# Kernel optimization log

Hardware: AMD Instinct MI355X
Metric: run time of the kernel (lower is better)

## Reference

```python
import jax, jax.numpy as jnp
import numpy as np

B, CIN, COUT, H, W = 64, 64, 64, 32, 32
K, STRIDE, PAD = 3, 1, 1
HOUT = (H + 2 * PAD - K) // STRIDE + 1
WOUT = (W + 2 * PAD - K) // STRIDE + 1


def setup_inputs() -> dict:
    key = jax.random.key(0)
    k1, k2, k3 = jax.random.split(key, 3)
    x = jax.random.normal(k1, (B, CIN, H, W), dtype=jnp.float32)
    # weight: per-location filters (leading singleton batch dim of the torch
    # param is dropped; it only served broadcasting)
    weight = jax.random.normal(k2, (CIN, COUT, HOUT, WOUT, K, K), dtype=jnp.float32)
    bias = jax.random.normal(k3, (COUT, HOUT, WOUT), dtype=jnp.float32)
    return {"x": x, "weight": weight, "bias": bias}


def _extract_patches(x, k, stride, pad, hout, wout):
    # x: [B, C, H, W] -> patches [B, C, k*k, hout, wout]
    xp = jnp.pad(x, ((0, 0), (0, 0), (pad, pad), (pad, pad)))
    slabs = [
        xp[:, :, i : i + (hout - 1) * stride + 1 : stride,
               j : j + (wout - 1) * stride + 1 : stride]
        for i in range(k) for j in range(k)
    ]
    return jnp.stack(slabs, axis=2)


def reference(x, weight, bias):
    cin, cout, hout, wout, k, _ = weight.shape
    patches = _extract_patches(x, k, STRIDE, PAD, hout, wout)  # [B, Cin, k*k, Ho, Wo]
    w = weight.reshape(cin, cout, hout, wout, k * k)
    # fused per-location dot product: avoids the [B,Cin,Cout,Ho,Wo,k,k] intermediate
    y = jnp.einsum('bikhw,iohwk->bohw', patches, w) + bias[None]
    return y
```

## Files before the change

### kernel.cpp

```cpp
#include <hip/hip_runtime.h>
#include <hip/hip_bf16.h>


#define B_    64
#define HW_   32
#define HP_   34
#define NLOC  1024
#define W_OST 9216u
#define W_IST 589824u
#define XT_BYTES  ((size_t)64*HP_*HP_*64*2)
#define WS_NEED   (XT_BYTES)
#define SCR_R 528

typedef __attribute__((ext_vector_type(8))) short short8;
typedef __attribute__((ext_vector_type(8))) unsigned short ushort8;
typedef __attribute__((ext_vector_type(4))) float floatx4;

static __device__ __forceinline__ unsigned short f2bf(float f) {
  __hip_bfloat16 h = __float2bfloat16(f);
  return __builtin_bit_cast(unsigned short, h);
}

static __device__ __forceinline__ void soft_barrier() {
  __asm__ volatile("s_waitcnt lgkmcnt(0)" ::: "memory");
  __builtin_amdgcn_s_barrier();
}

__global__ __launch_bounds__(256) void xpose_pad(const float* __restrict__ x,
                                                 unsigned short* __restrict__ xt) {
  int bid = blockIdx.x;
  int i = bid / HP_, hh = bid % HP_;
  __shared__ float tile[B_ * 33];
  int t = threadIdx.x;
  bool interior = (hh >= 1 && hh <= HW_);
  if (interior) {
    int h = hh - 1, w = t & 31, bs = t >> 5;
    #pragma unroll
    for (int r = 0; r < 8; ++r) {
      int b = r * 8 + bs;
      tile[b * 33 + w] = x[(((size_t)b * 64 + i) * HW_ + h) * HW_ + w];
    }
  }
  __syncthreads();
  int b = t & 63, wsb = t >> 6;
  size_t base = (size_t)(i * HP_ + hh) * HP_ * B_;
  #pragma unroll
  for (int s = 0; s < 9; ++s) {
    int ww = s * 4 + wsb;
    if (ww < HP_) {
      float v = 0.f;
      if (interior && ww >= 1 && ww <= HW_) v = tile[b * 33 + (ww - 1)];
      xt[base + (size_t)ww * B_ + b] = f2bf(v);
    }
  }
}

__global__ __launch_bounds__(256, 2) void lc2d_fused(
    const unsigned short* __restrict__ xt,
    const float* __restrict__ wsrc,
    const float* __restrict__ bias,
    float* __restrict__ out) {
  __shared__ __align__(16) unsigned short Bf[2][8 * 64 * 8];
  __shared__ __align__(16) unsigned short Bs[16 * 64 * 8];
  __shared__ __align__(16) unsigned short scr4[4][4 * SCR_R];

  const int bid   = blockIdx.x;
  const int lt    = ((bid & 7) << 6) | (bid >> 3);
  const int ohalf = lt & 1;
  const int loc0  = (lt >> 1) << 2;
  const int tid   = threadIdx.x;
  const int lane  = tid & 63;
  const int ll    = tid >> 6;
  const int loc   = loc0 + ll;
  const int hblk  = loc >> 5, wblk = loc & 31;
  const int col   = lane & 15;
  const int quad  = lane >> 4;
  const int o_0   = ohalf * 32 + col;

  floatx4 acc[4][2];
  {
    float b0 = bias[(unsigned)o_0 * 1024u + (unsigned)loc];
    float b1 = bias[(unsigned)(o_0 + 16) * 1024u + (unsigned)loc];
    #pragma unroll
    for (int mt = 0; mt < 4; ++mt) {
      acc[mt][0] = (floatx4){b0, b0, b0, b0};
      acc[mt][1] = (floatx4){b1, b1, b1, b1};
    }
  }

  floatx4 wa[5], wb[5];
  const bool lastok = (tid < 128);
  const size_t wrow = (size_t)loc0 * 9;
  const unsigned obase = (unsigned)ohalf * 32u;

  auto issueW = [&](int c, floatx4 (&wreg)[5]) {
    const int i0 = c << 2;
    #pragma unroll
    for (int r = 0; r < 5; ++r) {
      if (r < 4 || lastok) {
        int idx = r * 256 + tid;
        int g = idx / 9, p = idx - g * 9;
        int i = i0 + (g >> 5), o = (int)obase + (g & 31);
        wreg[r] = *(const floatx4*)(wsrc + (size_t)i * W_IST + (size_t)o * W_OST
                                    + wrow + (size_t)(p * 4));
      }
    }
  };
  auto scatterW = [&](int c, floatx4 (&wreg)[5], unsigned short* bfp) {
    const int i0 = c << 2;
    #pragma unroll
    for (int r = 0; r < 5; ++r) {
      if (r < 4 || lastok) {
        int idx = r * 256 + tid;
        int g = idx / 9, p = idx - g * 9;
        int iq = g >> 5, ol = g & 31;
        int ot = ol >> 4, oc = ol & 15;
        int flane = iq * 16 + oc;
        #pragma unroll
        for (int e = 0; e < 4; ++e) {
          int fi = p * 4 + e;
          int lle = fi / 9, kk = fi - lle * 9;
          unsigned short v = f2bf(wreg[r][e]);
          if (kk < 8) {
            bfp[((lle * 2 + ot) * 64 + flane) * 8 + kk] = v;
          } else {
            int i = i0 + iq;
            int sc = i >> 5, k2 = i & 31;
            Bs[(((lle * 2 + sc) * 2 + ot) * 64 + (k2 >> 3) * 16 + oc) * 8 + (k2 & 7)] = v;
          }
        }
      }
    }
  };

  auto xtLoad = [&](int t, int q) -> ushort8 {
    int i, kh, kw;
    if (t < 16) {
      i = (t << 2) + q;
      int kk = lane >> 3;
      kh = kk / 3; kw = kk - kh * 3;
    } else {
      i = ((t - 16) << 5) + (q << 3) + (lane >> 3);
      kh = 2; kw = 2;
    }
    return *(const ushort8*)(xt +
        (((unsigned)i * HP_ + (unsigned)(hblk + kh)) * HP_ + (unsigned)(wblk + kw)) * 64u
        + ((unsigned)(lane & 7) << 3));
  };

  auto buildA = [&](ushort8 v0, ushort8 v1, ushort8 v2, ushort8 v3,
                    ushort8 &a0, ushort8 &a1, ushort8 &a2, ushort8 &a3) {
    *(ushort8*)&scr4[ll][0 * SCR_R + (lane << 3)] = v0;
    *(ushort8*)&scr4[ll][1 * SCR_R + (lane << 3)] = v1;
    *(ushort8*)&scr4[ll][2 * SCR_R + (lane << 3)] = v2;
    *(ushort8*)&scr4[ll][3 * SCR_R + (lane << 3)] = v3;
    __asm__ volatile("s_waitcnt lgkmcnt(0)" ::: "memory");
    const int rb = (lane >> 4) * SCR_R + (lane & 15);
    #pragma unroll
    for (int j = 0; j < 8; ++j) {
      a0[j] = scr4[ll][rb + j * 64 +  0];
      a1[j] = scr4[ll][rb + j * 64 + 16];
      a2[j] = scr4[ll][rb + j * 64 + 32];
      a3[j] = scr4[ll][rb + j * 64 + 48];
    }
  };

  auto doMFMA = [&](ushort8 a0, ushort8 a1, ushort8 a2, ushort8 a3,
                    const unsigned short* bbase, int boff) {
    ushort8 b0 = *(const ushort8*)(bbase + (size_t)((boff + 0) * 64 + lane) * 8);
    ushort8 b1 = *(const ushort8*)(bbase + (size_t)((boff + 1) * 64 + lane) * 8);
    acc[0][0] = __builtin_amdgcn_mfma_f32_16x16x32_bf16(
        __builtin_bit_cast(short8, a0), __builtin_bit_cast(short8, b0), acc[0][0], 0, 0, 0);
    acc[1][0] = __builtin_amdgcn_mfma_f32_16x16x32_bf16(
        __builtin_bit_cast(short8, a1), __builtin_bit_cast(short8, b0), acc[1][0], 0, 0, 0);
    acc[2][0] = __builtin_amdgcn_mfma_f32_16x16x32_bf16(
        __builtin_bit_cast(short8, a2), __builtin_bit_cast(short8, b0), acc[2][0], 0, 0, 0);
    acc[3][0] = __builtin_amdgcn_mfma_f32_16x16x32_bf16(
        __builtin_bit_cast(short8, a3), __builtin_bit_cast(short8, b0), acc[3][0], 0, 0, 0);
    acc[0][1] = __builtin_amdgcn_mfma_f32_16x16x32_bf16(
        __builtin_bit_cast(short8, a0), __builtin_bit_cast(short8, b1), acc[0][1], 0, 0, 0);
    acc[1][1] = __builtin_amdgcn_mfma_f32_16x16x32_bf16(
        __builtin_bit_cast(short8, a1), __builtin_bit_cast(short8, b1), acc[1][1], 0, 0, 0);
    acc[2][1] = __builtin_amdgcn_mfma_f32_16x16x32_bf16(
        __builtin_bit_cast(short8, a2), __builtin_bit_cast(short8, b1), acc[2][1], 0, 0, 0);
    acc[3][1] = __builtin_amdgcn_mfma_f32_16x16x32_bf16(
        __builtin_bit_cast(short8, a3), __builtin_bit_cast(short8, b1), acc[3][1], 0, 0, 0);
  };

  issueW(0, wa);
  ushort8 a0, a1, a2, a3;
  {
    ushort8 xv0 = xtLoad(0, 0), xv1 = xtLoad(0, 1);
    ushort8 xv2 = xtLoad(0, 2), xv3 = xtLoad(0, 3);
    scatterW(0, wa, &Bf[0][0]);
    issueW(1, wb);
    buildA(xv0, xv1, xv2, xv3, a0, a1, a2, a3);
  }
  soft_barrier();

#define STEP(C, WI, WS) do {                                                  \
    const int c_ = (C);                                                       \
    ushort8 nx0 = xtLoad(c_ + 1, 0), nx1 = xtLoad(c_ + 1, 1);                 \
    ushort8 nx2 = xtLoad(c_ + 1, 2), nx3 = xtLoad(c_ + 1, 3);                 \
    if (c_ + 2 <= 15) issueW(c_ + 2, WI);                                     \
    doMFMA(a0, a1, a2, a3, &Bf[c_ & 1][0], ll << 1);                          \
    buildA(nx0, nx1, nx2, nx3, a0, a1, a2, a3);               \
    if (c_ + 1 <= 15) scatterW(c_ + 1, WS, &Bf[(c_ & 1) ^ 1][0]);             \
    soft_barrier();                                                           \
  } while (0)

  #pragma unroll 1
  for (int cc = 0; cc < 16; cc += 2) {
    STEP(cc,     wa, wb);
    STEP(cc + 1, wb, wa);
  }
#undef STEP

  {
    ushort8 nx0 = xtLoad(17, 0), nx1 = xtLoad(17, 1);
    ushort8 nx2 = xtLoad(17, 2), nx3 = xtLoad(17, 3);
    doMFMA(a0, a1, a2, a3, &Bs[0], (ll << 1) << 1);
    buildA(nx0, nx1, nx2, nx3, a0, a1, a2, a3);
    doMFMA(a0, a1, a2, a3, &Bs[0], ((ll << 1) + 1) << 1);
  }

  #pragma unroll
  for (int mt = 0; mt < 4; ++mt) {
    int b = mt * 16 + quad * 4;
    #pragma unroll
    for (int r = 0; r < 4; ++r) {
      out[((unsigned)(b + r) * 64u + (unsigned)o_0) * 1024u + (unsigned)loc] = acc[mt][0][r];
      out[((unsigned)(b + r) * 64u + (unsigned)(o_0 + 16)) * 1024u + (unsigned)loc] = acc[mt][1][r];
    }
  }
}

__global__ __launch_bounds__(256, 4) void lc2d_fallback(
    const float* __restrict__ x, const float* __restrict__ weight,
    const float* __restrict__ bias, float* __restrict__ out) {
  int t0 = blockIdx.x;
  int loc = ((t0 & 7) << 7) | (t0 >> 3);
  int h = loc >> 5, w = loc & 31;
  int tid = threadIdx.x;
  int b = tid & 63;
  int o0 = (tid >> 6) * 16;
  __shared__ float As[72 * 64];
  float acc[16];
  #pragma unroll
  for (int j = 0; j < 16; ++j) acc[j] = bias[(size_t)(o0 + j) * NLOC + loc];
  for (int ic = 0; ic < 8; ++ic) {
    __syncthreads();
    #pragma unroll
    for (int s = 0; s < 18; ++s) {
      int f = s * 256 + tid;
      int k = f >> 6, lb = f & 63;
      int kk = k >> 3, isub = k & 7;
      int i = ic * 8 + isub;
      int kh = kk / 3, kw = kk - kh * 3;
      int hh = h + kh - 1, ww = w + kw - 1;
      float v = (hh >= 0 && hh < HW_ && ww >= 0 && ww < HW_)
                  ? x[(((size_t)lb * 64 + i) * HW_ + hh) * HW_ + ww] : 0.f;
      As[k * 64 + lb] = v;
    }
    __syncthreads();
    #pragma unroll 1
    for (int isub = 0; isub < 8; ++isub) {
      const float* wp = weight + (size_t)(ic * 8 + isub) * W_IST
                               + (size_t)o0 * W_OST + loc * 9;
      #pragma unroll
      for (int kk = 0; kk < 9; ++kk) {
        float a = As[(kk * 8 + isub) * 64 + b];
        #pragma unroll
        for (int j = 0; j < 16; ++j)
          acc[j] = fmaf(a, wp[(size_t)j * W_OST + kk], acc[j]);
      }
    }
  }
  size_t ob = ((size_t)b * 64 + o0) * NLOC + loc;
  #pragma unroll
  for (int j = 0; j < 16; ++j) out[ob + (size_t)j * NLOC] = acc[j];
}

extern "C" void kernel_launch(void* const* d_in, const int* in_sizes, int n_in,
                              void* d_out, int out_size, void* d_ws, size_t ws_size,
                              hipStream_t stream) {
  const float* x  = (const float*)d_in[0];
  const float* wt = (const float*)d_in[1];
  const float* bs = (const float*)d_in[2];
  float* out = (float*)d_out;

  if (ws_size >= WS_NEED) {
    unsigned short* xtb = (unsigned short*)d_ws;
    xpose_pad<<<64 * HP_, 256, 0, stream>>>(x, xtb);
    lc2d_fused<<<512, 256, 0, stream>>>(xtb, wt, bs, out);
  } else {
    lc2d_fallback<<<NLOC, 256, 0, stream>>>(x, wt, bs, out);
  }
}
```

Measured before the change: 252.5 us.

## Load weight B-fragments directly into registers, dropping LDS staging and barriers

Each lane now loads its own 9 weight floats per (input channel, output) pair from global memory with unaligned 16-byte loads and converts them to bf16 MFMA B operands in registers. This removes the cooperative weight scatter into a shared double buffer and the per-step block barrier. Only the ninth tap is still written to shared memory for the tail MFMAs. In exchange, global weight loads become less coalesced and unaligned, and the barrier before the tail is replaced by a wave-local lgkmcnt wait.

Result: slower. 267.2 us (+5.8%).

```diff
diff --git a/kernel.cpp b/kernel.cpp
--- a/kernel.cpp
+++ b/kernel.cpp
@@ -21,9 +21,8 @@
   return __builtin_bit_cast(unsigned short, h);
 }
 
-static __device__ __forceinline__ void soft_barrier() {
-  __asm__ volatile("s_waitcnt lgkmcnt(0)" ::: "memory");
-  __builtin_amdgcn_s_barrier();
+static __device__ __forceinline__ floatx4 ldf4u(const float* p) {
+  floatx4 v; __builtin_memcpy(&v, p, 16); return v;
 }
 
 __global__ __launch_bounds__(256) void xpose_pad(const float* __restrict__ x,
@@ -60,7 +59,6 @@
     const float* __restrict__ wsrc,
     const float* __restrict__ bias,
     float* __restrict__ out) {
-  __shared__ __align__(16) unsigned short Bf[2][8 * 64 * 8];
   __shared__ __align__(16) unsigned short Bs[16 * 64 * 8];
   __shared__ __align__(16) unsigned short scr4[4][4 * SCR_R];
 
@@ -88,49 +86,31 @@
     }
   }
 
-  floatx4 wa[5], wb[5];
-  const bool lastok = (tid < 128);
-  const size_t wrow = (size_t)loc0 * 9;
-  const unsigned obase = (unsigned)ohalf * 32u;
-
-  auto issueW = [&](int c, floatx4 (&wreg)[5]) {
-    const int i0 = c << 2;
-    #pragma unroll
-    for (int r = 0; r < 5; ++r) {
-      if (r < 4 || lastok) {
-        int idx = r * 256 + tid;
-        int g = idx / 9, p = idx - g * 9;
-        int i = i0 + (g >> 5), o = (int)obase + (g & 31);
-        wreg[r] = *(const floatx4*)(wsrc + (size_t)i * W_IST + (size_t)o * W_OST
-                                    + wrow + (size_t)(p * 4));
-      }
-    }
-  };
-  auto scatterW = [&](int c, floatx4 (&wreg)[5], unsigned short* bfp) {
-    const int i0 = c << 2;
-    #pragma unroll
-    for (int r = 0; r < 5; ++r) {
-      if (r < 4 || lastok) {
-        int idx = r * 256 + tid;
-        int g = idx / 9, p = idx - g * 9;
-        int iq = g >> 5, ol = g & 31;
-        int ot = ol >> 4, oc = ol & 15;
-        int flane = iq * 16 + oc;
-        #pragma unroll
-        for (int e = 0; e < 4; ++e) {
-          int fi = p * 4 + e;
-          int lle = fi / 9, kk = fi - lle * 9;
-          unsigned short v = f2bf(wreg[r][e]);
-          if (kk < 8) {
-            bfp[((lle * 2 + ot) * 64 + flane) * 8 + kk] = v;
-          } else {
-            int i = i0 + iq;
-            int sc = i >> 5, k2 = i & 31;
-            Bs[(((lle * 2 + sc) * 2 + ot) * 64 + (k2 >> 3) * 16 + oc) * 8 + (k2 & 7)] = v;
-          }
-        }
-      }
-    }
+  const unsigned bbase0 = (unsigned)quad * W_IST + (unsigned)o_0 * W_OST
+                        + (unsigned)loc * 9u;
+  auto loadB = [&](int c, floatx4 &f0a, floatx4 &f0b, float &s0,
+                   floatx4 &f1a, floatx4 &f1b, float &s1) {
+    unsigned off = bbase0 + (unsigned)(4 * c) * W_IST;
+    f0a = ldf4u(wsrc + off);
+    f0b = ldf4u(wsrc + off + 4);
+    s0  = wsrc[off + 8];
+    unsigned off1 = off + 16u * W_OST;
+    f1a = ldf4u(wsrc + off1);
+    f1b = ldf4u(wsrc + off1 + 4);
+    s1  = wsrc[off1 + 8];
+  };
+  auto cvtB = [&](floatx4 fa, floatx4 fb) -> ushort8 {
+    ushort8 r;
+    r[0] = f2bf(fa[0]); r[1] = f2bf(fa[1]); r[2] = f2bf(fa[2]); r[3] = f2bf(fa[3]);
+    r[4] = f2bf(fb[0]); r[5] = f2bf(fb[1]); r[6] = f2bf(fb[2]); r[7] = f2bf(fb[3]);
+    return r;
+  };
+  auto stashB = [&](int c, float s0, float s1) {
+    int sc = c >> 3, cpr = c & 7;
+    int sub = (cpr >> 1) * 16 + col;
+    int el  = (cpr & 1) * 4 + quad;
+    Bs[(((ll * 2 + sc) * 2 + 0) * 64 + sub) * 8 + el] = f2bf(s0);
+    Bs[(((ll * 2 + sc) * 2 + 1) * 64 + sub) * 8 + el] = f2bf(s1);
   };
 
   auto xtLoad = [&](int t, int q) -> ushort8 {
@@ -147,7 +127,6 @@
         (((unsigned)i * HP_ + (unsigned)(hblk + kh)) * HP_ + (unsigned)(wblk + kw)) * 64u
         + ((unsigned)(lane & 7) << 3));
   };
-
   auto buildA = [&](ushort8 v0, ushort8 v1, ushort8 v2, ushort8 v3,
                     ushort8 &a0, ushort8 &a1, ushort8 &a2, ushort8 &a3) {
     *(ushort8*)&scr4[ll][0 * SCR_R + (lane << 3)] = v0;
@@ -166,9 +145,7 @@
   };
 
   auto doMFMA = [&](ushort8 a0, ushort8 a1, ushort8 a2, ushort8 a3,
-                    const unsigned short* bbase, int boff) {
-    ushort8 b0 = *(const ushort8*)(bbase + (size_t)((boff + 0) * 64 + lane) * 8);
-    ushort8 b1 = *(const ushort8*)(bbase + (size_t)((boff + 1) * 64 + lane) * 8);
+                    ushort8 b0, ushort8 b1) {
     acc[0][0] = __builtin_amdgcn_mfma_f32_16x16x32_bf16(
         __builtin_bit_cast(short8, a0), __builtin_bit_cast(short8, b0), acc[0][0], 0, 0, 0);
     acc[1][0] = __builtin_amdgcn_mfma_f32_16x16x32_bf16(
@@ -187,41 +164,47 @@
         __builtin_bit_cast(short8, a3), __builtin_bit_cast(short8, b1), acc[3][1], 0, 0, 0);
   };
 
-  issueW(0, wa);
-  ushort8 a0, a1, a2, a3;
-  {
-    ushort8 xv0 = xtLoad(0, 0), xv1 = xtLoad(0, 1);
-    ushort8 xv2 = xtLoad(0, 2), xv3 = xtLoad(0, 3);
-    scatterW(0, wa, &Bf[0][0]);
-    issueW(1, wb);
+  floatx4 cf0a, cf0b, cf1a, cf1b; float cs0, cs1;
+  floatx4 nf0a, nf0b, nf1a, nf1b; float ns0, ns1;
+  loadB(0, cf0a, cf0b, cs0, cf1a, cf1b, cs1);
+  ushort8 xv0 = xtLoad(0, 0), xv1 = xtLoad(0, 1);
+  ushort8 xv2 = xtLoad(0, 2), xv3 = xtLoad(0, 3);
+
+  #pragma unroll 1
+  for (int c = 0; c < 16; ++c) {
+    ushort8 nx0 = xtLoad(c + 1, 0), nx1 = xtLoad(c + 1, 1);
+    ushort8 nx2 = xtLoad(c + 1, 2), nx3 = xtLoad(c + 1, 3);
+    if (c < 15) loadB(c + 1, nf0a, nf0b, ns0, nf1a, nf1b, ns1);
+    ushort8 b0 = cvtB(cf0a, cf0b);
+    ushort8 b1 = cvtB(cf1a, cf1b);
+    stashB(c, cs0, cs1);
+    ushort8 a0, a1, a2, a3;
     buildA(xv0, xv1, xv2, xv3, a0, a1, a2, a3);
-  }
-  soft_barrier();
-
-#define STEP(C, WI, WS) do {                                                  \
-    const int c_ = (C);                                                       \
-    ushort8 nx0 = xtLoad(c_ + 1, 0), nx1 = xtLoad(c_ + 1, 1);                 \
-    ushort8 nx2 = xtLoad(c_ + 1, 2), nx3 = xtLoad(c_ + 1, 3);                 \
-    if (c_ + 2 <= 15) issueW(c_ + 2, WI);                                     \
-    doMFMA(a0, a1, a2, a3, &Bf[c_ & 1][0], ll << 1);                          \
-    buildA(nx0, nx1, nx2, nx3, a0, a1, a2, a3);               \
-    if (c_ + 1 <= 15) scatterW(c_ + 1, WS, &Bf[(c_ & 1) ^ 1][0]);             \
-    soft_barrier();                                                           \
-  } while (0)
-
-  #pragma unroll 1
-  for (int cc = 0; cc < 16; cc += 2) {
-    STEP(cc,     wa, wb);
-    STEP(cc + 1, wb, wa);
-  }
-#undef STEP
-
+    doMFMA(a0, a1, a2, a3, b0, b1);
+    cf0a = nf0a; cf0b = nf0b; cs0 = ns0;
+    cf1a = nf1a; cf1b = nf1b; cs1 = ns1;
+    xv0 = nx0; xv1 = nx1; xv2 = nx2; xv3 = nx3;
+  }
+
+  __asm__ volatile("s_waitcnt lgkmcnt(0)" ::: "memory");
   {
     ushort8 nx0 = xtLoad(17, 0), nx1 = xtLoad(17, 1);
     ushort8 nx2 = xtLoad(17, 2), nx3 = xtLoad(17, 3);
-    doMFMA(a0, a1, a2, a3, &Bs[0], (ll << 1) << 1);
+    ushort8 a0, a1, a2, a3;
+    buildA(xv0, xv1, xv2, xv3, a0, a1, a2, a3);
+    {
+      int boff = (ll << 1) << 1;
+      ushort8 b0 = *(const ushort8*)(&Bs[0] + (size_t)((boff + 0) * 64 + lane) * 8);
+      ushort8 b1 = *(const ushort8*)(&Bs[0] + (size_t)((boff + 1) * 64 + lane) * 8);
+      doMFMA(a0, a1, a2, a3, b0, b1);
+    }
     buildA(nx0, nx1, nx2, nx3, a0, a1, a2, a3);
-    doMFMA(a0, a1, a2, a3, &Bs[0], ((ll << 1) + 1) << 1);
+    {
+      int boff = ((ll << 1) + 1) << 1;
+      ushort8 b0 = *(const ushort8*)(&Bs[0] + (size_t)((boff + 0) * 64 + lane) * 8);
+      ushort8 b1 = *(const ushort8*)(&Bs[0] + (size_t)((boff + 1) * 64 + lane) * 8);
+      doMFMA(a0, a1, a2, a3, b0, b1);
+    }
   }
 
   #pragma unroll
```

## Split output channels into quarter tiles and double block count

Applied to the files above, without the earlier changes.

Each block now computes 16 output channels for 4 locations instead of 32, and the grid grows from 512 to 1024 blocks. Per-block weight staging, accumulators and LDS shrink by half, which lowers register and shared-memory pressure and gives more blocks for latency hiding. The cost is that each block repeats the input patch loads and the A-fragment shuffle, doubling activation reads and LDS transpose work relative to the useful MFMA count.

New measurement: 265.9 us. +5.3%, slower.

```diff
diff --git a/kernel.cpp b/kernel.cpp
--- a/kernel.cpp
+++ b/kernel.cpp
@@ -60,14 +60,14 @@
     const float* __restrict__ wsrc,
     const float* __restrict__ bias,
     float* __restrict__ out) {
-  __shared__ __align__(16) unsigned short Bf[2][8 * 64 * 8];
-  __shared__ __align__(16) unsigned short Bs[16 * 64 * 8];
+  __shared__ __align__(16) unsigned short Bf[2][4 * 64 * 8];
+  __shared__ __align__(16) unsigned short Bs[8 * 64 * 8];
   __shared__ __align__(16) unsigned short scr4[4][4 * SCR_R];
 
   const int bid   = blockIdx.x;
-  const int lt    = ((bid & 7) << 6) | (bid >> 3);
-  const int ohalf = lt & 1;
-  const int loc0  = (lt >> 1) << 2;
+  const int lt    = ((bid & 7) << 7) | (bid >> 3);
+  const int oq    = lt & 3;
+  const int loc0  = (lt >> 2) << 2;
   const int tid   = threadIdx.x;
   const int lane  = tid & 63;
   const int ll    = tid >> 6;
@@ -75,46 +75,41 @@
   const int hblk  = loc >> 5, wblk = loc & 31;
   const int col   = lane & 15;
   const int quad  = lane >> 4;
-  const int o_0   = ohalf * 32 + col;
-
-  floatx4 acc[4][2];
+  const int o_0   = oq * 16 + col;
+
+  floatx4 acc[4];
   {
     float b0 = bias[(unsigned)o_0 * 1024u + (unsigned)loc];
-    float b1 = bias[(unsigned)(o_0 + 16) * 1024u + (unsigned)loc];
-    #pragma unroll
-    for (int mt = 0; mt < 4; ++mt) {
-      acc[mt][0] = (floatx4){b0, b0, b0, b0};
-      acc[mt][1] = (floatx4){b1, b1, b1, b1};
-    }
-  }
-
-  floatx4 wa[5], wb[5];
-  const bool lastok = (tid < 128);
+    #pragma unroll
+    for (int mt = 0; mt < 4; ++mt) acc[mt] = (floatx4){b0, b0, b0, b0};
+  }
+
+  floatx4 wa[3], wb[3];
+  const bool lastok = (tid < 64);
   const size_t wrow = (size_t)loc0 * 9;
-  const unsigned obase = (unsigned)ohalf * 32u;
-
-  auto issueW = [&](int c, floatx4 (&wreg)[5]) {
+  const unsigned obase = (unsigned)oq * 16u;
+
+  auto issueW = [&](int c, floatx4 (&wreg)[3]) {
     const int i0 = c << 2;
     #pragma unroll
-    for (int r = 0; r < 5; ++r) {
-      if (r < 4 || lastok) {
+    for (int r = 0; r < 3; ++r) {
+      if (r < 2 || lastok) {
         int idx = r * 256 + tid;
         int g = idx / 9, p = idx - g * 9;
-        int i = i0 + (g >> 5), o = (int)obase + (g & 31);
+        int i = i0 + (g >> 4), o = (int)obase + (g & 15);
         wreg[r] = *(const floatx4*)(wsrc + (size_t)i * W_IST + (size_t)o * W_OST
                                     + wrow + (size_t)(p * 4));
       }
     }
   };
-  auto scatterW = [&](int c, floatx4 (&wreg)[5], unsigned short* bfp) {
+  auto scatterW = [&](int c, floatx4 (&wreg)[3], unsigned short* bfp) {
     const int i0 = c << 2;
     #pragma unroll
-    for (int r = 0; r < 5; ++r) {
-      if (r < 4 || lastok) {
+    for (int r = 0; r < 3; ++r) {
+      if (r < 2 || lastok) {
         int idx = r * 256 + tid;
         int g = idx / 9, p = idx - g * 9;
-        int iq = g >> 5, ol = g & 31;
-        int ot = ol >> 4, oc = ol & 15;
+        int iq = g >> 4, oc = g & 15;
         int flane = iq * 16 + oc;
         #pragma unroll
         for (int e = 0; e < 4; ++e) {
@@ -122,11 +117,11 @@
           int lle = fi / 9, kk = fi - lle * 9;
           unsigned short v = f2bf(wreg[r][e]);
           if (kk < 8) {
-            bfp[((lle * 2 + ot) * 64 + flane) * 8 + kk] = v;
+            bfp[(lle * 64 + flane) * 8 + kk] = v;
           } else {
             int i = i0 + iq;
             int sc = i >> 5, k2 = i & 31;
-            Bs[(((lle * 2 + sc) * 2 + ot) * 64 + (k2 >> 3) * 16 + oc) * 8 + (k2 & 7)] = v;
+            Bs[((lle * 2 + sc) * 64 + (k2 >> 3) * 16 + oc) * 8 + (k2 & 7)] = v;
           }
         }
       }
@@ -147,7 +142,6 @@
         (((unsigned)i * HP_ + (unsigned)(hblk + kh)) * HP_ + (unsigned)(wblk + kw)) * 64u
         + ((unsigned)(lane & 7) << 3));
   };
-
   auto buildA = [&](ushort8 v0, ushort8 v1, ushort8 v2, ushort8 v3,
                     ushort8 &a0, ushort8 &a1, ushort8 &a2, ushort8 &a3) {
     *(ushort8*)&scr4[ll][0 * SCR_R + (lane << 3)] = v0;
@@ -165,26 +159,15 @@
     }
   };
 
-  auto doMFMA = [&](ushort8 a0, ushort8 a1, ushort8 a2, ushort8 a3,
-                    const unsigned short* bbase, int boff) {
-    ushort8 b0 = *(const ushort8*)(bbase + (size_t)((boff + 0) * 64 + lane) * 8);
-    ushort8 b1 = *(const ushort8*)(bbase + (size_t)((boff + 1) * 64 + lane) * 8);
-    acc[0][0] = __builtin_amdgcn_mfma_f32_16x16x32_bf16(
-        __builtin_bit_cast(short8, a0), __builtin_bit_cast(short8, b0), acc[0][0], 0, 0, 0);
-    acc[1][0] = __builtin_amdgcn_mfma_f32_16x16x32_bf16(
-        __builtin_bit_cast(short8, a1), __builtin_bit_cast(short8, b0), acc[1][0], 0, 0, 0);
-    acc[2][0] = __builtin_amdgcn_mfma_f32_16x16x32_bf16(
-        __builtin_bit_cast(short8, a2), __builtin_bit_cast(short8, b0), acc[2][0], 0, 0, 0);
-    acc[3][0] = __builtin_amdgcn_mfma_f32_16x16x32_bf16(
-        __builtin_bit_cast(short8, a3), __builtin_bit_cast(short8, b0), acc[3][0], 0, 0, 0);
-    acc[0][1] = __builtin_amdgcn_mfma_f32_16x16x32_bf16(
-        __builtin_bit_cast(short8, a0), __builtin_bit_cast(short8, b1), acc[0][1], 0, 0, 0);
-    acc[1][1] = __builtin_amdgcn_mfma_f32_16x16x32_bf16(
-        __builtin_bit_cast(short8, a1), __builtin_bit_cast(short8, b1), acc[1][1], 0, 0, 0);
-    acc[2][1] = __builtin_amdgcn_mfma_f32_16x16x32_bf16(
-        __builtin_bit_cast(short8, a2), __builtin_bit_cast(short8, b1), acc[2][1], 0, 0, 0);
-    acc[3][1] = __builtin_amdgcn_mfma_f32_16x16x32_bf16(
-        __builtin_bit_cast(short8, a3), __builtin_bit_cast(short8, b1), acc[3][1], 0, 0, 0);
+  auto doMFMA = [&](ushort8 a0, ushort8 a1, ushort8 a2, ushort8 a3, ushort8 b0) {
+    acc[0] = __builtin_amdgcn_mfma_f32_16x16x32_bf16(
+        __builtin_bit_cast(short8, a0), __builtin_bit_cast(short8, b0), acc[0], 0, 0, 0);
+    acc[1] = __builtin_amdgcn_mfma_f32_16x16x32_bf16(
+        __builtin_bit_cast(short8, a1), __builtin_bit_cast(short8, b0), acc[1], 0, 0, 0);
+    acc[2] = __builtin_amdgcn_mfma_f32_16x16x32_bf16(
+        __builtin_bit_cast(short8, a2), __builtin_bit_cast(short8, b0), acc[2], 0, 0, 0);
+    acc[3] = __builtin_amdgcn_mfma_f32_16x16x32_bf16(
+        __builtin_bit_cast(short8, a3), __builtin_bit_cast(short8, b0), acc[3], 0, 0, 0);
   };
 
   issueW(0, wa);
@@ -203,7 +186,9 @@
     ushort8 nx0 = xtLoad(c_ + 1, 0), nx1 = xtLoad(c_ + 1, 1);                 \
     ushort8 nx2 = xtLoad(c_ + 1, 2), nx3 = xtLoad(c_ + 1, 3);                 \
     if (c_ + 2 <= 15) issueW(c_ + 2, WI);                                     \
-    doMFMA(a0, a1, a2, a3, &Bf[c_ & 1][0], ll << 1);                          \
+    ushort8 b0 = *(const ushort8*)(&Bf[c_ & 1][0]                             \
+                                   + (size_t)(ll * 64 + lane) * 8);           \
+    doMFMA(a0, a1, a2, a3, b0);                                               \
     buildA(nx0, nx1, nx2, nx3, a0, a1, a2, a3);               \
     if (c_ + 1 <= 15) scatterW(c_ + 1, WS, &Bf[(c_ & 1) ^ 1][0]);             \
     soft_barrier();                                                           \
@@ -219,9 +204,15 @@
   {
     ushort8 nx0 = xtLoad(17, 0), nx1 = xtLoad(17, 1);
     ushort8 nx2 = xtLoad(17, 2), nx3 = xtLoad(17, 3);
-    doMFMA(a0, a1, a2, a3, &Bs[0], (ll << 1) << 1);
+    {
+      ushort8 b0 = *(const ushort8*)(&Bs[0] + (size_t)(((ll << 1) + 0) * 64 + lane) * 8);
+      doMFMA(a0, a1, a2, a3, b0);
+    }
     buildA(nx0, nx1, nx2, nx3, a0, a1, a2, a3);
-    doMFMA(a0, a1, a2, a3, &Bs[0], ((ll << 1) + 1) << 1);
+    {
+      ushort8 b0 = *(const ushort8*)(&Bs[0] + (size_t)(((ll << 1) + 1) * 64 + lane) * 8);
+      doMFMA(a0, a1, a2, a3, b0);
+    }
   }
 
   #pragma unroll
@@ -229,8 +220,7 @@
     int b = mt * 16 + quad * 4;
     #pragma unroll
     for (int r = 0; r < 4; ++r) {
-      out[((unsigned)(b + r) * 64u + (unsigned)o_0) * 1024u + (unsigned)loc] = acc[mt][0][r];
-      out[((unsigned)(b + r) * 64u + (unsigned)(o_0 + 16)) * 1024u + (unsigned)loc] = acc[mt][1][r];
+      out[((unsigned)(b + r) * 64u + (unsigned)o_0) * 1024u + (unsigned)loc] = acc[mt][r];
     }
   }
 }
@@ -292,7 +282,7 @@
   if (ws_size >= WS_NEED) {
     unsigned short* xtb = (unsigned short*)d_ws;
     xpose_pad<<<64 * HP_, 256, 0, stream>>>(x, xtb);
-    lc2d_fused<<<512, 256, 0, stream>>>(xtb, wt, bs, out);
+    lc2d_fused<<<1024, 256, 0, stream>>>(xtb, wt, bs, out);
   } else {
     lc2d_fallback<<<NLOC, 256, 0, stream>>>(x, wt, bs, out);
   }
```
